# Kernel optimization log

Measured on AMD Instinct MI355X. Metric: run time of the kernel, lower is better.

The kernel has to match this reference:

```python
import jax, jax.numpy as jnp
import numpy as np
from jax import lax

V_WORD, D_WORD = 50000, 300
V_CHAR, D_CHAR = 128, 50
FILTER_NUM, KSIZE = 4, 3
OUT_CH = D_CHAR * FILTER_NUM  # 200
SENT, BATCH, WLEN = 256, 64, 16


def setup_inputs() -> dict:
    key = jax.random.key(0)
    k1, k2, k3, k4, k5, k6 = jax.random.split(key, 6)
    words = jax.random.randint(k1, (SENT, BATCH), 0, V_WORD, dtype=jnp.int32)
    chars = jax.random.randint(k2, (BATCH, SENT, WLEN), 0, V_CHAR, dtype=jnp.int32)
    W_word = jax.random.normal(k3, (V_WORD, D_WORD), dtype=jnp.float32) * 0.1
    W_char = jax.random.normal(k4, (V_CHAR, D_CHAR), dtype=jnp.float32) * 0.1
    conv_w = jax.random.normal(k5, (OUT_CH, D_CHAR, KSIZE), dtype=jnp.float32) * 0.1
    conv_b = jax.random.normal(k6, (OUT_CH,), dtype=jnp.float32) * 0.1
    return {"words": words, "chars": chars, "W_word": W_word, "W_char": W_char,
            "conv_w": conv_w, "conv_b": conv_b}


def reference(words, chars, W_word, W_char, conv_w, conv_b):
    # word embedding: [S, B, Dw]  (dropout layers are identity in eval mode)
    word_emb = W_word[words]
    # char embedding: [B, S, L, Dc]
    char_emb = W_char[chars]
    B, S, L, Dc = char_emb.shape
    # batch all words into one conv call: [B*S, Dc, L]
    x = char_emb.reshape(B * S, L, Dc).transpose(0, 2, 1)
    y = lax.conv_general_dilated(
        x, conv_w, window_strides=(1,), padding='VALID',
        dimension_numbers=('NCH', 'OIH', 'NCH'))  # [B*S, OUT_CH, L-K+1]
    y = y + conv_b[None, :, None]
    pooled = jnp.max(y, axis=2).reshape(B, S, -1)  # [B, S, OUT_CH]
    char_feat = pooled.transpose(1, 0, 2)          # [S, B, OUT_CH]
    return jnp.concatenate([word_emb, char_feat], axis=2)  # [S, B, Dw+OUT_CH]
```

## Files before the change

### kernel.cpp

```cpp
#include <hip/hip_runtime.h>

#define SENT    256
#define BATCH   64
#define WLEN    16
#define D_WORDE 300
#define D_CHARE 50
#define OUT_CH  200
#define KSIZE   3
#define NPOS    14
#define D_OUT   500
#define NWORDS  (SENT * BATCH)

#define KPAD      192
#define MPAD      208
#define CHARP_U16 (129 * 64)
#define WO_U16    (MPAD * KPAD)
#define WS_NEED   ((size_t)(CHARP_U16 + WO_U16) * 2)

#define WPB         16
#define TILE_U16    (WPB * 1024)
#define CONV_BLOCKS (NWORDS / WPB)

typedef short  short8  __attribute__((ext_vector_type(8)));
typedef ushort ushort8 __attribute__((ext_vector_type(8)));
typedef float  float4v __attribute__((ext_vector_type(4)));

#define GLOAD16(SRC, DST)                                                     \
    __builtin_amdgcn_global_load_lds(                                         \
        (const __attribute__((address_space(1))) void*)(SRC),                 \
        (__attribute__((address_space(3))) void*)(DST), 16, 0, 0)

__device__ __forceinline__ ushort f2bf(float f) {
    unsigned u = __float_as_uint(f);
    u = (u + 0x7FFFu + ((u >> 16) & 1u)) >> 16;
    return (ushort)u;
}

__global__ void prep_kernel(const float* __restrict__ W_char,
                            const float* __restrict__ conv_w,
                            const float* __restrict__ conv_b,
                            ushort* __restrict__ ws) {
    int j = blockIdx.x * 256 + threadIdx.x;
    if (j < CHARP_U16) {
        int r = j >> 6, c = j & 63;
        ushort v = 0;
        if (r < 128) {
            if (c < D_CHARE)      v = f2bf(W_char[r * D_CHARE + c]);
            else if (c == 63)     v = 0x3F80;
        }
        ws[j] = v;
    }
    int j2 = j - CHARP_U16;
    if (j2 >= 0 && j2 < WO_U16) {
        int o = j2 / KPAD, kg = j2 - o * KPAD;
        int kk = kg >> 6, c = kg & 63;
        float v = 0.f;
        if (o < OUT_CH) {
            if (c < D_CHARE)      v = conv_w[o * (D_CHARE * KSIZE) + c * KSIZE + kk];
            else if (kg == 191)   v = conv_b[o];
        }
        ws[CHARP_U16 + j2] = f2bf(v);
    }
}

__device__ __forceinline__ float4v fmax4(float4v a, float4v b) {
    float4v r;
    r[0] = fmaxf(a[0], b[0]); r[1] = fmaxf(a[1], b[1]);
    r[2] = fmaxf(a[2], b[2]); r[3] = fmaxf(a[3], b[3]);
    return r;
}

__device__ __forceinline__ short8 lda(const ushort* __restrict__ tile,
                                      int l15, int row, int g) {
    int pos = g ^ (row & 7) ^ (l15 & 7);
    return *(const short8*)&tile[l15 * 1024 + row * 64 + (pos << 3)];
}

template <int NT>
__device__ __forceinline__ void conv_ploop(int tbase, int lane, int l15, int lg,
                                           const ushort* __restrict__ tile,
                                           const ushort* __restrict__ WO,
                                           float* __restrict__ out, int block0) {
    short8 B[NT][6];
    #pragma unroll
    for (int i = 0; i < NT; i++) {
        int col = (tbase + i) * 16 + l15;
        #pragma unroll
        for (int s = 0; s < 6; s++)
            B[i][s] = *(const short8*)&WO[col * KPAD + s * 32 + lg * 8];
    }

    short8 w[8];
    #pragma unroll
    for (int rr = 0; rr < 4; rr++) {
        w[rr * 2]     = lda(tile, l15, rr, lg);
        w[rr * 2 + 1] = lda(tile, l15, rr, 4 + lg);
    }

    float4v mx[NT];
    #pragma unroll
    for (int pp = 0; pp < 7; pp++) {
        float4v ap[NT], aq[NT];
        #pragma unroll
        for (int i = 0; i < NT; i++) { ap[i] = (float4v){0,0,0,0}; aq[i] = (float4v){0,0,0,0}; }
        #pragma unroll
        for (int s = 0; s < 6; s++) {
            #pragma unroll
            for (int i = 0; i < NT; i++) {
                ap[i] = __builtin_amdgcn_mfma_f32_16x16x32_bf16(w[s],     B[i][s], ap[i], 0, 0, 0);
                aq[i] = __builtin_amdgcn_mfma_f32_16x16x32_bf16(w[s + 2], B[i][s], aq[i], 0, 0, 0);
            }
        }
        #pragma unroll
        for (int i = 0; i < NT; i++) {
            float4v m2 = fmax4(ap[i], aq[i]);
            mx[i] = (pp == 0) ? m2 : fmax4(mx[i], m2);
        }
        if (pp < 6) {
            #pragma unroll
            for (int j = 0; j < 4; j++) w[j] = w[j + 4];
            const int r0 = 2 * pp + 4;
            w[4] = lda(tile, l15, r0,     lg);
            w[5] = lda(tile, l15, r0,     4 + lg);
            w[6] = lda(tile, l15, r0 + 1, lg);
            w[7] = lda(tile, l15, r0 + 1, 4 + lg);
        }
    }

    #pragma unroll
    for (int i = 0; i < NT; i++) {
        int col = (tbase + i) * 16 + l15;
        if (col < OUT_CH) {
            #pragma unroll
            for (int j = 0; j < 4; j++)
                out[(size_t)(block0 + lg * 4 + j) * D_OUT + D_WORDE + col] = mx[i][j];
        }
    }
}

__global__ void __launch_bounds__(512)
fused_kernel(const int* __restrict__ words, const int* __restrict__ chars,
             const float* __restrict__ W_word, const ushort* __restrict__ ws,
             float* __restrict__ out) {
    __shared__ __align__(16) ushort tile[TILE_U16];

    const int tid  = threadIdx.x;
    const int lane = tid & 63;
    const int wave = tid >> 6;
    const int l15  = lane & 15;
    const int lg   = lane >> 4;

    const ushort* __restrict__ charP = ws;
    const ushort* __restrict__ WO    = ws + CHARP_U16;
    const int block0 = blockIdx.x * WPB;

    #pragma unroll
    for (int ww = 0; ww < 2; ww++) {
        const int wl = wave * 2 + ww;
        const int m  = block0 + wl;
        const int* __restrict__ cbase = chars + ((m & 63) * SENT + (m >> 6)) * WLEN;
        const int srcg = (lane & 7) ^ ((lane >> 3) & 7) ^ (wl & 7);
        #pragma unroll
        for (int s = 0; s < 2; s++) {
            const int idv = cbase[s * 8 + (lane >> 3)];
            GLOAD16(charP + idv * 64 + (srcg << 3), &tile[wl * 1024 + s * 512]);
        }
    }
    __syncthreads();

    if (wave < 6) {
        conv_ploop<2>(2 * wave, lane, l15, lg, tile, WO, out, block0);
    } else if (wave == 6) {
        conv_ploop<1>(12, lane, l15, lg, tile, WO, out, block0);
    } else {
        const bool tail = lane < (75 - 64);
        #pragma unroll 1
        for (int r4 = 0; r4 < 4; r4++) {
            const int m0 = block0 + r4 * 4;
            float4v e0[4], e1[4];
            #pragma unroll
            for (int j = 0; j < 4; j++) {
                const float4v* __restrict__ src =
                    (const float4v*)(W_word + (size_t)words[m0 + j] * D_WORDE);
                e0[j] = src[lane];
                e1[j] = tail ? src[64 + lane] : (float4v){0, 0, 0, 0};
            }
            #pragma unroll
            for (int j = 0; j < 4; j++) {
                float4v* __restrict__ dst = (float4v*)(out + (size_t)(m0 + j) * D_OUT);
                dst[lane] = e0[j];
                if (tail) dst[64 + lane] = e1[j];
            }
        }
    }
}

__global__ void __launch_bounds__(256)
word_emb_kernel(const int* __restrict__ words, const float* __restrict__ W_word,
                float* __restrict__ out) {
    int wave = threadIdx.x >> 6, lane = threadIdx.x & 63;
    int m = blockIdx.x * 4 + wave;
    int idx = words[m];
    const float* __restrict__ src = W_word + (size_t)idx * D_WORDE;
    float* __restrict__ dst = out + (size_t)m * D_OUT;
    for (int j = lane; j < D_WORDE; j += 64) dst[j] = src[j];
}

__global__ void __launch_bounds__(256)
char_conv_f32_kernel(const int* __restrict__ chars, const float* __restrict__ W_char,
                     const float* __restrict__ conv_w, const float* __restrict__ conv_b,
                     float* __restrict__ out) {
    __shared__ __align__(16) float xs[D_CHARE * WLEN];
    __shared__ int ids[WLEN];
    int m = blockIdx.x, s = m >> 6, b = m & 63, tid = threadIdx.x;
    if (tid < WLEN) ids[tid] = chars[(b * SENT + s) * WLEN + tid];
    __syncthreads();
    for (int e = tid; e < D_CHARE * WLEN; e += 256) {
        int c = e >> 4, l = e & 15;
        xs[e] = W_char[ids[l] * D_CHARE + c];
    }
    __syncthreads();
    if (tid < OUT_CH) {
        float acc[NPOS];
        #pragma unroll
        for (int p = 0; p < NPOS; p++) acc[p] = 0.f;
        const float4* xs4 = (const float4*)xs;
        for (int c = 0; c < D_CHARE; c++) {
            float4 a0 = xs4[c*4+0], a1 = xs4[c*4+1], a2 = xs4[c*4+2], a3 = xs4[c*4+3];
            float xr[WLEN] = {a0.x,a0.y,a0.z,a0.w, a1.x,a1.y,a1.z,a1.w,
                              a2.x,a2.y,a2.z,a2.w, a3.x,a3.y,a3.z,a3.w};
            #pragma unroll
            for (int k = 0; k < KSIZE; k++) {
                float wv = conv_w[tid * (D_CHARE * KSIZE) + c * KSIZE + k];
                #pragma unroll
                for (int p = 0; p < NPOS; p++) acc[p] = fmaf(wv, xr[p + k], acc[p]);
            }
        }
        float mx = acc[0];
        #pragma unroll
        for (int p = 1; p < NPOS; p++) mx = fmaxf(mx, acc[p]);
        out[(size_t)m * D_OUT + D_WORDE + tid] = mx + conv_b[tid];
    }
}

extern "C" void kernel_launch(void* const* d_in, const int* in_sizes, int n_in,
                              void* d_out, int out_size, void* d_ws, size_t ws_size,
                              hipStream_t stream) {
    const int*   words  = (const int*)d_in[0];
    const int*   chars  = (const int*)d_in[1];
    const float* W_word = (const float*)d_in[2];
    const float* W_char = (const float*)d_in[3];
    const float* conv_w = (const float*)d_in[4];
    const float* conv_b = (const float*)d_in[5];
    float* out = (float*)d_out;

    if (ws_size >= WS_NEED) {
        ushort* ws = (ushort*)d_ws;
        hipLaunchKernelGGL(prep_kernel,
                           dim3((CHARP_U16 + WO_U16 + 255) / 256), dim3(256), 0, stream,
                           W_char, conv_w, conv_b, ws);
        hipLaunchKernelGGL(fused_kernel, dim3(CONV_BLOCKS), dim3(512), 0, stream,
                           words, chars, W_word, ws, out);
    } else {
        hipLaunchKernelGGL(word_emb_kernel, dim3(NWORDS / 4), dim3(256), 0, stream,
                           words, W_word, out);
        hipLaunchKernelGGL(char_conv_f32_kernel, dim3(NWORDS), dim3(256), 0, stream,
                           chars, W_char, conv_w, conv_b, out);
    }
}
```

Baseline: 33.14 us.

## Split char-tile gather into two halves and overlap second half with conv compute

Result: slower. 34.66 us (+4.6%).

```diff
diff --git a/kernel.cpp b/kernel.cpp
--- a/kernel.cpp
+++ b/kernel.cpp
@@ -77,29 +77,37 @@
 }
 
 template <int NT>
-__device__ __forceinline__ void conv_ploop(int tbase, int lane, int l15, int lg,
-                                           const ushort* __restrict__ tile,
-                                           const ushort* __restrict__ WO,
-                                           float* __restrict__ out, int block0) {
-    short8 B[NT][6];
+struct ConvState {
+    short8  B[NT][6];
+    short8  w[8];
+    float4v mx[NT];
+};
+
+template <int NT>
+__device__ __forceinline__ void conv_init(ConvState<NT>& st, int tbase,
+                                          int l15, int lg,
+                                          const ushort* __restrict__ WO) {
     #pragma unroll
     for (int i = 0; i < NT; i++) {
         int col = (tbase + i) * 16 + l15;
         #pragma unroll
         for (int s = 0; s < 6; s++)
-            B[i][s] = *(const short8*)&WO[col * KPAD + s * 32 + lg * 8];
-    }
-
-    short8 w[8];
-    #pragma unroll
-    for (int rr = 0; rr < 4; rr++) {
-        w[rr * 2]     = lda(tile, l15, rr, lg);
-        w[rr * 2 + 1] = lda(tile, l15, rr, 4 + lg);
-    }
-
-    float4v mx[NT];
-    #pragma unroll
-    for (int pp = 0; pp < 7; pp++) {
+            st.B[i][s] = *(const short8*)&WO[col * KPAD + s * 32 + lg * 8];
+    }
+}
+
+template <int NT, int PP0, int PP1>
+__device__ __forceinline__ void conv_run(ConvState<NT>& st, int l15, int lg,
+                                         const ushort* __restrict__ tile) {
+    if (PP0 == 0) {
+        #pragma unroll
+        for (int rr = 0; rr < 4; rr++) {
+            st.w[rr * 2]     = lda(tile, l15, rr, lg);
+            st.w[rr * 2 + 1] = lda(tile, l15, rr, 4 + lg);
+        }
+    }
+    #pragma unroll
+    for (int pp = PP0; pp < PP1; pp++) {
         float4v ap[NT], aq[NT];
         #pragma unroll
         for (int i = 0; i < NT; i++) { ap[i] = (float4v){0,0,0,0}; aq[i] = (float4v){0,0,0,0}; }
@@ -107,33 +115,38 @@
         for (int s = 0; s < 6; s++) {
             #pragma unroll
             for (int i = 0; i < NT; i++) {
-                ap[i] = __builtin_amdgcn_mfma_f32_16x16x32_bf16(w[s],     B[i][s], ap[i], 0, 0, 0);
-                aq[i] = __builtin_amdgcn_mfma_f32_16x16x32_bf16(w[s + 2], B[i][s], aq[i], 0, 0, 0);
+                ap[i] = __builtin_amdgcn_mfma_f32_16x16x32_bf16(st.w[s],     st.B[i][s], ap[i], 0, 0, 0);
+                aq[i] = __builtin_amdgcn_mfma_f32_16x16x32_bf16(st.w[s + 2], st.B[i][s], aq[i], 0, 0, 0);
             }
         }
         #pragma unroll
         for (int i = 0; i < NT; i++) {
             float4v m2 = fmax4(ap[i], aq[i]);
-            mx[i] = (pp == 0) ? m2 : fmax4(mx[i], m2);
+            st.mx[i] = (pp == 0) ? m2 : fmax4(st.mx[i], m2);
         }
         if (pp < 6) {
             #pragma unroll
-            for (int j = 0; j < 4; j++) w[j] = w[j + 4];
+            for (int j = 0; j < 4; j++) st.w[j] = st.w[j + 4];
             const int r0 = 2 * pp + 4;
-            w[4] = lda(tile, l15, r0,     lg);
-            w[5] = lda(tile, l15, r0,     4 + lg);
-            w[6] = lda(tile, l15, r0 + 1, lg);
-            w[7] = lda(tile, l15, r0 + 1, 4 + lg);
-        }
-    }
-
+            st.w[4] = lda(tile, l15, r0,     lg);
+            st.w[5] = lda(tile, l15, r0,     4 + lg);
+            st.w[6] = lda(tile, l15, r0 + 1, lg);
+            st.w[7] = lda(tile, l15, r0 + 1, 4 + lg);
+        }
+    }
+}
+
+template <int NT>
+__device__ __forceinline__ void conv_store(const ConvState<NT>& st, int tbase,
+                                           int l15, int lg,
+                                           float* __restrict__ out, int block0) {
     #pragma unroll
     for (int i = 0; i < NT; i++) {
         int col = (tbase + i) * 16 + l15;
         if (col < OUT_CH) {
             #pragma unroll
             for (int j = 0; j < 4; j++)
-                out[(size_t)(block0 + lg * 4 + j) * D_OUT + D_WORDE + col] = mx[i][j];
+                out[(size_t)(block0 + lg * 4 + j) * D_OUT + D_WORDE + col] = st.mx[i][j];
         }
     }
 }
@@ -154,28 +167,72 @@
     const ushort* __restrict__ WO    = ws + CHARP_U16;
     const int block0 = blockIdx.x * WPB;
 
+    int ids_[2];
+    int srcg_[2];
     #pragma unroll
     for (int ww = 0; ww < 2; ww++) {
         const int wl = wave * 2 + ww;
         const int m  = block0 + wl;
         const int* __restrict__ cbase = chars + ((m & 63) * SENT + (m >> 6)) * WLEN;
-        const int srcg = (lane & 7) ^ ((lane >> 3) & 7) ^ (wl & 7);
-        #pragma unroll
-        for (int s = 0; s < 2; s++) {
-            const int idv = cbase[s * 8 + (lane >> 3)];
-            GLOAD16(charP + idv * 64 + (srcg << 3), &tile[wl * 1024 + s * 512]);
-        }
+        srcg_[ww] = (lane & 7) ^ ((lane >> 3) & 7) ^ (wl & 7);
+        ids_[ww] = cbase[(lane >> 3)];
+    }
+    #pragma unroll
+    for (int ww = 0; ww < 2; ww++) {
+        const int wl = wave * 2 + ww;
+        GLOAD16(charP + ids_[ww] * 64 + (srcg_[ww] << 3), &tile[wl * 1024]);
+    }
+    int ids1_[2];
+    #pragma unroll
+    for (int ww = 0; ww < 2; ww++) {
+        const int m = block0 + wave * 2 + ww;
+        ids1_[ww] = chars[((m & 63) * SENT + (m >> 6)) * WLEN + 8 + (lane >> 3)];
     }
     __syncthreads();
 
+    #pragma unroll
+    for (int ww = 0; ww < 2; ww++) {
+        const int wl = wave * 2 + ww;
+        GLOAD16(charP + ids1_[ww] * 64 + (srcg_[ww] << 3), &tile[wl * 1024 + 512]);
+    }
+
     if (wave < 6) {
-        conv_ploop<2>(2 * wave, lane, l15, lg, tile, WO, out, block0);
+        ConvState<2> st;
+        conv_init<2>(st, 2 * wave, l15, lg, WO);
+        conv_run<2, 0, 2>(st, l15, lg, tile);
+        __syncthreads();
+        conv_run<2, 2, 7>(st, l15, lg, tile);
+        conv_store<2>(st, 2 * wave, l15, lg, out, block0);
     } else if (wave == 6) {
-        conv_ploop<1>(12, lane, l15, lg, tile, WO, out, block0);
+        ConvState<1> st;
+        conv_init<1>(st, 12, l15, lg, WO);
+        conv_run<1, 0, 2>(st, l15, lg, tile);
+        __syncthreads();
+        conv_run<1, 2, 7>(st, l15, lg, tile);
+        conv_store<1>(st, 12, l15, lg, out, block0);
     } else {
         const bool tail = lane < (75 - 64);
         #pragma unroll 1
-        for (int r4 = 0; r4 < 4; r4++) {
+        for (int r4 = 0; r4 < 2; r4++) {
+            const int m0 = block0 + r4 * 4;
+            float4v e0[4], e1[4];
+            #pragma unroll
+            for (int j = 0; j < 4; j++) {
+                const float4v* __restrict__ src =
+                    (const float4v*)(W_word + (size_t)words[m0 + j] * D_WORDE);
+                e0[j] = src[lane];
+                e1[j] = tail ? src[64 + lane] : (float4v){0, 0, 0, 0};
+            }
+            #pragma unroll
+            for (int j = 0; j < 4; j++) {
+                float4v* __restrict__ dst = (float4v*)(out + (size_t)(m0 + j) * D_OUT);
+                dst[lane] = e0[j];
+                if (tail) dst[64 + lane] = e1[j];
+            }
+        }
+        __syncthreads();
+        #pragma unroll 1
+        for (int r4 = 2; r4 < 4; r4++) {
             const int m0 = block0 + r4 * 4;
             float4v e0[4], e1[4];
             #pragma unroll
```

## Use 1024-thread blocks with one conv column tile per wave

Applied to the files above, without the earlier changes.

Result: slower. 110.3 us (+232.8%).

```diff
diff --git a/kernel.cpp b/kernel.cpp
--- a/kernel.cpp
+++ b/kernel.cpp
@@ -76,69 +76,7 @@
     return *(const short8*)&tile[l15 * 1024 + row * 64 + (pos << 3)];
 }
 
-template <int NT>
-__device__ __forceinline__ void conv_ploop(int tbase, int lane, int l15, int lg,
-                                           const ushort* __restrict__ tile,
-                                           const ushort* __restrict__ WO,
-                                           float* __restrict__ out, int block0) {
-    short8 B[NT][6];
-    #pragma unroll
-    for (int i = 0; i < NT; i++) {
-        int col = (tbase + i) * 16 + l15;
-        #pragma unroll
-        for (int s = 0; s < 6; s++)
-            B[i][s] = *(const short8*)&WO[col * KPAD + s * 32 + lg * 8];
-    }
-
-    short8 w[8];
-    #pragma unroll
-    for (int rr = 0; rr < 4; rr++) {
-        w[rr * 2]     = lda(tile, l15, rr, lg);
-        w[rr * 2 + 1] = lda(tile, l15, rr, 4 + lg);
-    }
-
-    float4v mx[NT];
-    #pragma unroll
-    for (int pp = 0; pp < 7; pp++) {
-        float4v ap[NT], aq[NT];
-        #pragma unroll
-        for (int i = 0; i < NT; i++) { ap[i] = (float4v){0,0,0,0}; aq[i] = (float4v){0,0,0,0}; }
-        #pragma unroll
-        for (int s = 0; s < 6; s++) {
-            #pragma unroll
-            for (int i = 0; i < NT; i++) {
-                ap[i] = __builtin_amdgcn_mfma_f32_16x16x32_bf16(w[s],     B[i][s], ap[i], 0, 0, 0);
-                aq[i] = __builtin_amdgcn_mfma_f32_16x16x32_bf16(w[s + 2], B[i][s], aq[i], 0, 0, 0);
-            }
-        }
-        #pragma unroll
-        for (int i = 0; i < NT; i++) {
-            float4v m2 = fmax4(ap[i], aq[i]);
-            mx[i] = (pp == 0) ? m2 : fmax4(mx[i], m2);
-        }
-        if (pp < 6) {
-            #pragma unroll
-            for (int j = 0; j < 4; j++) w[j] = w[j + 4];
-            const int r0 = 2 * pp + 4;
-            w[4] = lda(tile, l15, r0,     lg);
-            w[5] = lda(tile, l15, r0,     4 + lg);
-            w[6] = lda(tile, l15, r0 + 1, lg);
-            w[7] = lda(tile, l15, r0 + 1, 4 + lg);
-        }
-    }
-
-    #pragma unroll
-    for (int i = 0; i < NT; i++) {
-        int col = (tbase + i) * 16 + l15;
-        if (col < OUT_CH) {
-            #pragma unroll
-            for (int j = 0; j < 4; j++)
-                out[(size_t)(block0 + lg * 4 + j) * D_OUT + D_WORDE + col] = mx[i][j];
-        }
-    }
-}
-
-__global__ void __launch_bounds__(512)
+__global__ void __launch_bounds__(1024, 8)
 fused_kernel(const int* __restrict__ words, const int* __restrict__ chars,
              const float* __restrict__ W_word, const ushort* __restrict__ ws,
              float* __restrict__ out) {
@@ -154,42 +92,80 @@
     const ushort* __restrict__ WO    = ws + CHARP_U16;
     const int block0 = blockIdx.x * WPB;
 
-    #pragma unroll
-    for (int ww = 0; ww < 2; ww++) {
-        const int wl = wave * 2 + ww;
-        const int m  = block0 + wl;
+    {
+        const int m = block0 + wave;
         const int* __restrict__ cbase = chars + ((m & 63) * SENT + (m >> 6)) * WLEN;
-        const int srcg = (lane & 7) ^ ((lane >> 3) & 7) ^ (wl & 7);
-        #pragma unroll
-        for (int s = 0; s < 2; s++) {
-            const int idv = cbase[s * 8 + (lane >> 3)];
-            GLOAD16(charP + idv * 64 + (srcg << 3), &tile[wl * 1024 + s * 512]);
-        }
+        const int srcg = (lane & 7) ^ ((lane >> 3) & 7) ^ (wave & 7);
+        const int id0 = cbase[(lane >> 3)];
+        const int id1 = cbase[8 + (lane >> 3)];
+        GLOAD16(charP + id0 * 64 + (srcg << 3), &tile[wave * 1024]);
+        GLOAD16(charP + id1 * 64 + (srcg << 3), &tile[wave * 1024 + 512]);
     }
     __syncthreads();
 
-    if (wave < 6) {
-        conv_ploop<2>(2 * wave, lane, l15, lg, tile, WO, out, block0);
-    } else if (wave == 6) {
-        conv_ploop<1>(12, lane, l15, lg, tile, WO, out, block0);
+    if (wave < 13) {
+        short8 B[6];
+        const int col = wave * 16 + l15;
+        #pragma unroll
+        for (int s = 0; s < 6; s++)
+            B[s] = *(const short8*)&WO[col * KPAD + s * 32 + lg * 8];
+
+        short8 w[8];
+        #pragma unroll
+        for (int rr = 0; rr < 4; rr++) {
+            w[rr * 2]     = lda(tile, l15, rr, lg);
+            w[rr * 2 + 1] = lda(tile, l15, rr, 4 + lg);
+        }
+
+        float4v mx = {-3.4e38f, -3.4e38f, -3.4e38f, -3.4e38f};
+        #pragma unroll 1
+        for (int pp = 0; pp < 7; pp++) {
+            float4v ap = {0, 0, 0, 0}, aq = {0, 0, 0, 0};
+            #pragma unroll
+            for (int s = 0; s < 6; s++) {
+                ap = __builtin_amdgcn_mfma_f32_16x16x32_bf16(w[s],     B[s], ap, 0, 0, 0);
+                aq = __builtin_amdgcn_mfma_f32_16x16x32_bf16(w[s + 2], B[s], aq, 0, 0, 0);
+            }
+            mx = fmax4(mx, fmax4(ap, aq));
+            if (pp < 6) {
+                #pragma unroll
+                for (int j = 0; j < 4; j++) w[j] = w[j + 4];
+                const int r0 = 2 * pp + 4;
+                w[4] = lda(tile, l15, r0,     lg);
+                w[5] = lda(tile, l15, r0,     4 + lg);
+                w[6] = lda(tile, l15, r0 + 1, lg);
+                w[7] = lda(tile, l15, r0 + 1, 4 + lg);
+            }
+        }
+
+        if (col < OUT_CH) {
+            #pragma unroll
+            for (int j = 0; j < 4; j++)
+                out[(size_t)(block0 + lg * 4 + j) * D_OUT + D_WORDE + col] = mx[j];
+        }
     } else {
+        const int e = wave - 13;
         const bool tail = lane < (75 - 64);
         #pragma unroll 1
-        for (int r4 = 0; r4 < 4; r4++) {
-            const int m0 = block0 + r4 * 4;
-            float4v e0[4], e1[4];
-            #pragma unroll
-            for (int j = 0; j < 4; j++) {
-                const float4v* __restrict__ src =
-                    (const float4v*)(W_word + (size_t)words[m0 + j] * D_WORDE);
-                e0[j] = src[lane];
-                e1[j] = tail ? src[64 + lane] : (float4v){0, 0, 0, 0};
-            }
-            #pragma unroll
-            for (int j = 0; j < 4; j++) {
-                float4v* __restrict__ dst = (float4v*)(out + (size_t)(m0 + j) * D_OUT);
-                dst[lane] = e0[j];
-                if (tail) dst[64 + lane] = e1[j];
+        for (int r = e; r < 16; r += 6) {
+            const int m0 = block0 + r;
+            const bool two = (r + 3 < 16);
+            const int m1 = block0 + (two ? r + 3 : r);
+            const float4v* __restrict__ s0 =
+                (const float4v*)(W_word + (size_t)words[m0] * D_WORDE);
+            const float4v* __restrict__ s1 =
+                (const float4v*)(W_word + (size_t)words[m1] * D_WORDE);
+            float4v a0 = s0[lane];
+            float4v a1 = tail ? s0[64 + lane] : (float4v){0, 0, 0, 0};
+            float4v b0 = s1[lane];
+            float4v b1 = tail ? s1[64 + lane] : (float4v){0, 0, 0, 0};
+            float4v* __restrict__ d0 = (float4v*)(out + (size_t)m0 * D_OUT);
+            d0[lane] = a0;
+            if (tail) d0[64 + lane] = a1;
+            if (two) {
+                float4v* __restrict__ d1 = (float4v*)(out + (size_t)m1 * D_OUT);
+                d1[lane] = b0;
+                if (tail) d1[64 + lane] = b1;
             }
         }
     }
@@ -259,7 +235,7 @@
         hipLaunchKernelGGL(prep_kernel,
                            dim3((CHARP_U16 + WO_U16 + 255) / 256), dim3(256), 0, stream,
                            W_char, conv_w, conv_b, ws);
-        hipLaunchKernelGGL(fused_kernel, dim3(CONV_BLOCKS), dim3(512), 0, stream,
+        hipLaunchKernelGGL(fused_kernel, dim3(CONV_BLOCKS), dim3(1024), 0, stream,
                            words, chars, W_word, ws, out);
     } else {
         hipLaunchKernelGGL(word_emb_kernel, dim3(NWORDS / 4), dim3(256), 0, stream,
```
